# Kernel optimization log

Measured on AMD Instinct MI355X. Metric: run time of the kernel, lower is better.

The kernel has to match this reference:

```python
import jax, jax.numpy as jnp
import numpy as np

D_MODEL = 1024
NUM_HEADS = 16
HEAD_DIM = D_MODEL // NUM_HEADS


def setup_inputs() -> dict:
    key = jax.random.key(0)
    ks = jax.random.split(key, 9)
    B, S, D = 4, 2048, D_MODEL
    scale = 1.0 / np.sqrt(D)
    x = jax.random.normal(ks[0], (B, S, D), dtype=jnp.float32)
    wq = jax.random.normal(ks[1], (D, D), dtype=jnp.float32) * scale
    wk = jax.random.normal(ks[2], (D, D), dtype=jnp.float32) * scale
    wv = jax.random.normal(ks[3], (D, D), dtype=jnp.float32) * scale
    wo = jax.random.normal(ks[4], (D, D), dtype=jnp.float32) * scale
    bq = jax.random.normal(ks[5], (D,), dtype=jnp.float32) * 0.02
    bk = jax.random.normal(ks[6], (D,), dtype=jnp.float32) * 0.02
    bv = jax.random.normal(ks[7], (D,), dtype=jnp.float32) * 0.02
    bo = jax.random.normal(ks[8], (D,), dtype=jnp.float32) * 0.02
    return {"x": x, "wq": wq, "bq": bq, "wk": wk, "bk": bk,
            "wv": wv, "bv": bv, "wo": wo, "bo": bo}


def _split_heads(t):  # [B,S,D] -> [B,H,S,Dh]
    B, S, _ = t.shape
    return t.reshape(B, S, NUM_HEADS, HEAD_DIM).transpose(0, 2, 1, 3)


def reference(x, wq, bq, wk, bk, wv, bv, wo, bo):
    B, S, D = x.shape
    q = _split_heads(x @ wq + bq)  # [B,H,S,Dh]
    k = _split_heads(x @ wk + bk)
    v = _split_heads(x @ wv + bv)
    scores = jnp.einsum("bhqd,bhkd->bhqk", q, k) / jnp.sqrt(
        jnp.asarray(HEAD_DIM, dtype=x.dtype))
    causal = jnp.tril(jnp.ones((S, S), dtype=bool))  # [S,S]
    scores = jnp.where(causal, scores, jnp.finfo(scores.dtype).min)
    attn = jax.nn.softmax(scores, axis=-1)
    ctx = jnp.einsum("bhqk,bhkd->bhqd", attn, v)  # [B,H,S,Dh]
    ctx = ctx.transpose(0, 2, 1, 3).reshape(B, S, D)
    return ctx @ wo + bo
```

## Files before the change

### kernel.cpp

```cpp
#include <hip/hip_runtime.h>
#include <hip/hip_bf16.h>
#include <stdint.h>

#define DMODEL 1024
#define NH 16
#define DH 64
#define BATCH 4
#define SEQ 2048

#if __has_builtin(__builtin_amdgcn_exp2f)
#define EXP2F(x) __builtin_amdgcn_exp2f(x)
#else
#define EXP2F(x) exp2f(x)
#endif

typedef __attribute__((ext_vector_type(8))) short short8;
typedef __attribute__((ext_vector_type(4))) float f32x4;
typedef __attribute__((ext_vector_type(4))) ushort ushort4v;

__device__ __forceinline__ ushort f2bf(float f) {
    union { float f; unsigned u; } v; v.f = f;
    unsigned r = v.u + 0x7fffu + ((v.u >> 16) & 1u);
    return (ushort)(r >> 16);
}

__global__ __launch_bounds__(256) void convert_bf16(const float* __restrict__ src,
                                                    ushort* __restrict__ dst) {
    const size_t i = ((size_t)blockIdx.x * 256 + threadIdx.x) * 8;
    float4 a = *(const float4*)(src + i);
    float4 b = *(const float4*)(src + i + 4);
    short8 r;
    r[0] = (short)f2bf(a.x); r[1] = (short)f2bf(a.y);
    r[2] = (short)f2bf(a.z); r[3] = (short)f2bf(a.w);
    r[4] = (short)f2bf(b.x); r[5] = (short)f2bf(b.y);
    r[6] = (short)f2bf(b.z); r[7] = (short)f2bf(b.w);
    *(short8*)(dst + i) = r;
}

__global__ __launch_bounds__(256) void transpose_cvt_w4(
    const float* __restrict__ s0, const float* __restrict__ s1,
    const float* __restrict__ s2, const float* __restrict__ s3,
    ushort* __restrict__ d0, ushort* __restrict__ d1,
    ushort* __restrict__ d2, ushort* __restrict__ d3) {
    __shared__ ushort tile[64][65];
    const int z = blockIdx.z;
    const float* src = (z == 0) ? s0 : (z == 1) ? s1 : (z == 2) ? s2 : s3;
    ushort* dst = (z == 0) ? d0 : (z == 1) ? d1 : (z == 2) ? d2 : d3;
    const int bx = blockIdx.x * 64;
    const int by = blockIdx.y * 64;
    const int tx = threadIdx.x & 63, ty = threadIdx.x >> 6;
    #pragma unroll
    for (int i = 0; i < 64; i += 4)
        tile[ty + i][tx] = f2bf(src[(size_t)(by + ty + i) * DMODEL + bx + tx]);
    __syncthreads();
    #pragma unroll
    for (int i = 0; i < 64; i += 4)
        dst[(size_t)(bx + ty + i) * DMODEL + by + tx] = tile[tx][ty + i];
}

#define BK 64
#define NT 16

template <int MODE>
__global__ __launch_bounds__(512, 2) void gemm_tile(
    const ushort* __restrict__ A, const ushort* __restrict__ Bt,
    const float* __restrict__ b0, const float* __restrict__ b1,
    const float* __restrict__ b2,
    void* __restrict__ o0v, void* __restrict__ o1v, void* __restrict__ o2v) {
    __shared__ __align__(16) ushort lds[73728];
    const int tid  = threadIdx.x;
    const int lane = tid & 63;
    const int wv   = tid >> 6;

    const int bid = blockIdx.x;
    const int by  = 4 * (bid & 7) + ((bid >> 3) & 3);
    const int bx  = bid >> 5;
    const int mBase = by * 256, nBase = bx * 128;

    const int wm = (wv >> 1) * 64;
    const int wn = (wv & 1) * 64;
    const int frow = lane & 15;
    const int fq   = lane >> 4;
    const int r7   = frow & 7;
    const int sw0  = (fq ^ r7) << 3;
    const int sw1  = ((4 + fq) ^ r7) << 3;

    const int trow = tid >> 3;
    const int tcho = ((tid & 7) ^ (trow & 7)) * 8;
    const ushort* gA = A  + (size_t)(mBase + trow) * DMODEL + tcho;
    const ushort* gB = Bt + (size_t)(nBase + trow) * DMODEL + tcho;
    const int ldsw = wv * 512;

    f32x4 acc[4][4];
    #pragma unroll
    for (int i = 0; i < 4; ++i)
        #pragma unroll
        for (int j = 0; j < 4; ++j) acc[i][j] = (f32x4){0.f, 0.f, 0.f, 0.f};

#define STG(gp, off) __builtin_amdgcn_global_load_lds( \
    (const __attribute__((address_space(1))) void*)(gp), \
    (__attribute__((address_space(3))) void*)&lds[(off) + ldsw], 16, 0, 0)
#define STAGE_A(sb, u, h) STG(gA + (size_t)(h) * 64 * DMODEL + (u) * BK, \
                              (sb) + (h) * 4096)
#define STAGE_B(sb, u, h) STG(gB + (size_t)(h) * 64 * DMODEL + (u) * BK, \
                              (sb) + 16384 + (h) * 4096)

    STAGE_A(0, 0, 0); STAGE_A(0, 0, 1); STAGE_A(0, 0, 2); STAGE_A(0, 0, 3);
    STAGE_B(0, 0, 0); STAGE_B(0, 0, 1);
    STAGE_A(24576, 1, 0); STAGE_A(24576, 1, 1); STAGE_A(24576, 1, 2);
    STAGE_A(24576, 1, 3); STAGE_B(24576, 1, 0); STAGE_B(24576, 1, 1);
    asm volatile("s_waitcnt vmcnt(6)" ::: "memory");
    __builtin_amdgcn_s_barrier();

    int sc = 0;
    #pragma unroll 1
    for (int u = 0; u < NT; ++u) {
        const int scB = sc * 24576;
        const int sp  = (sc == 0) ? 2 : sc - 1;
        const int spB = sp * 24576;
        const ushort* bufA = &lds[scB + wm * 64];
        const ushort* bufB = &lds[scB + 16384 + wn * 64];

        short8 af[4][2], bf[2][2];

        #pragma unroll
        for (int f = 0; f < 4; ++f) {
            const int ro = (f * 16 + frow) * 64;
            af[f][0] = *(const short8*)&bufA[ro + sw0];
            af[f][1] = *(const short8*)&bufA[ro + sw1];
        }
        #pragma unroll
        for (int f2 = 0; f2 < 2; ++f2) {
            const int ro = (f2 * 16 + frow) * 64;
            bf[f2][0] = *(const short8*)&bufB[ro + sw0];
            bf[f2][1] = *(const short8*)&bufB[ro + sw1];
        }
        if (u + 2 < NT) {
            STAGE_A(spB, u + 2, 0); STAGE_A(spB, u + 2, 1); STAGE_A(spB, u + 2, 2);
        }
        __builtin_amdgcn_s_barrier();
        asm volatile("s_waitcnt lgkmcnt(0)" ::: "memory");
        __builtin_amdgcn_s_setprio(1);
        #pragma unroll
        for (int f = 0; f < 4; ++f)
            #pragma unroll
            for (int f2 = 0; f2 < 2; ++f2)
                #pragma unroll
                for (int ks = 0; ks < 2; ++ks)
                    acc[f][f2] = __builtin_amdgcn_mfma_f32_16x16x32_bf16(
                        af[f][ks], bf[f2][ks], acc[f][f2], 0, 0, 0);
        __builtin_amdgcn_s_setprio(0);
        __builtin_amdgcn_s_barrier();

        #pragma unroll
        for (int f2 = 0; f2 < 2; ++f2) {
            const int ro = (32 + f2 * 16 + frow) * 64;
            bf[f2][0] = *(const short8*)&bufB[ro + sw0];
            bf[f2][1] = *(const short8*)&bufB[ro + sw1];
        }
        if (u + 2 < NT) {
            STAGE_A(spB, u + 2, 3); STAGE_B(spB, u + 2, 0); STAGE_B(spB, u + 2, 1);
        }
        __builtin_amdgcn_s_barrier();
        asm volatile("s_waitcnt lgkmcnt(0)" ::: "memory");
        __builtin_amdgcn_s_setprio(1);
        #pragma unroll
        for (int f = 0; f < 4; ++f)
            #pragma unroll
            for (int f2 = 0; f2 < 2; ++f2)
                #pragma unroll
                for (int ks = 0; ks < 2; ++ks)
                    acc[f][2 + f2] = __builtin_amdgcn_mfma_f32_16x16x32_bf16(
                        af[f][ks], bf[f2][ks], acc[f][2 + f2], 0, 0, 0);
        __builtin_amdgcn_s_setprio(0);
        if (u + 2 < NT)       { asm volatile("s_waitcnt vmcnt(6)" ::: "memory"); }
        else if (u + 2 == NT) { asm volatile("s_waitcnt vmcnt(0)" ::: "memory"); }
        __builtin_amdgcn_s_barrier();
        sc = (sc == 2) ? 0 : sc + 1;
    }
#undef STG
#undef STAGE_A
#undef STAGE_B

    const int orow = fq * 4;
    const int ocol = frow;

    if (MODE == 1) {
        #pragma unroll
        for (int i = 0; i < 4; ++i)
            #pragma unroll
            for (int j = 0; j < 4; ++j)
                #pragma unroll
                for (int r = 0; r < 4; ++r) {
                    const int m = mBase + wm + i * 16 + orow + r;
                    const int n = nBase + wn + j * 16 + ocol;
                    ((float*)o0v)[(size_t)m * DMODEL + n] = acc[i][j][r] + b0[n];
                }
        return;
    }

    __syncthreads();
    ushort* o0 = (ushort*)o0v; ushort* o1 = (ushort*)o1v; ushort* o2 = (ushort*)o2v;
    ushort* sw = &lds[wv * 1152];
    const int mat = nBase >> 10;
    const int nb0 = (nBase & 1023) + wn;
    const int hb  = nb0 >> 6;
    const float* bp = (mat == 0) ? b0 : ((mat == 1) ? b1 : b2);
    float bj[4];
    #pragma unroll
    for (int j = 0; j < 4; ++j) bj[j] = bp[nb0 + j * 16 + ocol];
    const int mrow = mBase + wm;
    const int bbq = mrow >> 11;
    const int s0w = mrow & 2047;
    const float qscale = (mat == 0) ? 0.1803368801f : 1.0f;

    if (mat < 2) {
        ushort* obase = ((mat == 0) ? o0 : o1) +
                        ((size_t)(bbq * NH + hb) * SEQ + s0w) * DH;
        const int row = lane >> 2, cc = lane & 3;
        #pragma unroll
        for (int i = 0; i < 4; ++i) {
            #pragma unroll
            for (int j = 0; j < 4; ++j)
                #pragma unroll
                for (int r = 0; r < 4; ++r)
                    sw[(orow + r) * 72 + j * 16 + ocol] =
                        f2bf((acc[i][j][r] + bj[j]) * qscale);
            asm volatile("s_waitcnt lgkmcnt(0)" ::: "memory");
            #pragma unroll
            for (int p = 0; p < 2; ++p) {
                short8 v8 = *(const short8*)&sw[row * 72 + cc * 8 + p * 32];
                *(short8*)&obase[(size_t)(i * 16 + row) * DH + cc * 8 + p * 32] = v8;
            }
            asm volatile("s_waitcnt lgkmcnt(0)" ::: "memory");
        }
    } else {
        const int rowd = lane >> 2, scl = lane & 3;
        #pragma unroll
        for (int j = 0; j < 4; ++j) {
            #pragma unroll
            for (int ii = 0; ii < 4; ++ii)
                #pragma unroll
                for (int r = 0; r < 4; ++r)
                    sw[ocol * 72 + ii * 16 + orow + r] = f2bf(acc[ii][j][r] + bj[j]);
            asm volatile("s_waitcnt lgkmcnt(0)" ::: "memory");
            ushort* vbase = o2 + ((size_t)(bbq * NH + hb) * DH + j * 16 + rowd) * SEQ + s0w;
            #pragma unroll
            for (int p = 0; p < 2; ++p) {
                short8 v8 = *(const short8*)&sw[rowd * 72 + scl * 8 + p * 32];
                *(short8*)&vbase[scl * 8 + p * 32] = v8;
            }
            asm volatile("s_waitcnt lgkmcnt(0)" ::: "memory");
        }
    }
}

#define PSTR 72
__global__ __launch_bounds__(512, 6) void flash_attn(
    const ushort* __restrict__ Q, const ushort* __restrict__ K,
    const ushort* __restrict__ Vt, ushort* __restrict__ ctx) {
    __shared__ __align__(16) ushort Ks[2][4096];
    __shared__ __align__(16) ushort Vs[2][4096];
    __shared__ __align__(16) ushort plds[8][16 * PSTR];
    const int tid  = threadIdx.x;
    const int lane = tid & 63;
    const int wv   = tid >> 6;
    const int bh   = blockIdx.x & 63;
    const int Jp   = blockIdx.x >> 6;
    const int bb = bh >> 4, h = bh & 15;

    const ushort* Qb = Q + (size_t)bh * SEQ * DH;
    const ushort* Kb = K + (size_t)bh * SEQ * DH;
    const ushort* Vb = Vt + (size_t)bh * DH * SEQ;

    const int frow = lane & 15;
    const int fq   = lane >> 4;
    const int trow = tid >> 3;
    const int tcho = ((tid & 7) ^ (trow & 7)) * 8;
    const int ldsw = wv * 512;

    short8 ones;
    #pragma unroll
    for (int i = 0; i < 8; ++i) ones[i] = (short)0x3F80;

#define FA_STG(gp, lp) __builtin_amdgcn_global_load_lds( \
    (const __attribute__((address_space(1))) void*)(gp), \
    (__attribute__((address_space(3))) void*)(lp), 16, 0, 0)

    #pragma unroll 1
    for (int half = 0; half < 2; ++half) {
        const int J = half ? (15 - Jp) : Jp;
        const int ktmax = 2 * J + 1;
        const int q0 = J * 128 + (wv >> 2) * 64 + (wv & 3) * 16;
        const int qmax = q0 + 15;

        short8 qf[2];
        #pragma unroll
        for (int ks = 0; ks < 2; ++ks)
            qf[ks] = *(const short8*)&Qb[(size_t)(q0 + frow) * DH + ks * 32 + fq * 8];

        f32x4 o[4], lacc;
        #pragma unroll
        for (int t = 0; t < 4; ++t) o[t] = (f32x4){0.f, 0.f, 0.f, 0.f};
        lacc = (f32x4){0.f, 0.f, 0.f, 0.f};

        FA_STG(Kb + (size_t)trow * DH + tcho, &Ks[0][ldsw]);
        FA_STG(Vb + (size_t)trow * SEQ + tcho, &Vs[0][ldsw]);
        asm volatile("s_waitcnt vmcnt(0)" ::: "memory");
        __builtin_amdgcn_s_barrier();

        #pragma unroll 1
        for (int kt = 0; kt <= ktmax; ++kt) {
            const int k0 = kt * 64;
            const int cur = kt & 1;
            if (kt < ktmax) {
                const int kn = k0 + 64;
                FA_STG(Kb + (size_t)(kn + trow) * DH + tcho, &Ks[cur ^ 1][ldsw]);
                FA_STG(Vb + (size_t)trow * SEQ + kn + tcho, &Vs[cur ^ 1][ldsw]);
            }
            const ushort* Ksc = Ks[cur];
            const ushort* Vsc = Vs[cur];

            if (k0 <= qmax) {
            if (k0 + 64 <= q0) {
                f32x4 sacc[4];
                #pragma unroll
                for (int nt = 0; nt < 4; ++nt) sacc[nt] = (f32x4){0.f, 0.f, 0.f, 0.f};
                #pragma unroll
                for (int nt = 0; nt < 4; ++nt) {
                    const int row = nt * 16 + frow, r7 = row & 7;
                    #pragma unroll
                    for (int ks = 0; ks < 2; ++ks) {
                        short8 kf = *(const short8*)
                            &Ksc[(row >> 3) * 512 + r7 * 64 + (((ks * 4 + fq) ^ r7) * 8)];
                        sacc[nt] = __builtin_amdgcn_mfma_f32_16x16x32_bf16(kf, qf[ks],
                                                                          sacc[nt], 0, 0, 0);
                    }
                }
                #pragma unroll
                for (int nt = 0; nt < 4; ++nt) {
                    float p0 = EXP2F(sacc[nt][0]);
                    float p1 = EXP2F(sacc[nt][1]);
                    float p2 = EXP2F(sacc[nt][2]);
                    float p3 = EXP2F(sacc[nt][3]);
                    uint2 dw;
                    dw.x = __builtin_amdgcn_perm(__float_as_uint(p1), __float_as_uint(p0),
                                                 0x07060302u);
                    dw.y = __builtin_amdgcn_perm(__float_as_uint(p3), __float_as_uint(p2),
                                                 0x07060302u);
                    *(uint2*)&plds[wv][frow * PSTR + nt * 16 + fq * 4] = dw;
                }
                asm volatile("s_waitcnt lgkmcnt(0)" ::: "memory");
                #pragma unroll
                for (int kc = 0; kc < 2; ++kc) {
                    short8 pf = *(const short8*)&plds[wv][frow * PSTR + kc * 32 + fq * 8];
                    lacc = __builtin_amdgcn_mfma_f32_16x16x32_bf16(ones, pf, lacc, 0, 0, 0);
                    __builtin_amdgcn_s_setprio(1);
                    #pragma unroll
                    for (int t = 0; t < 4; ++t) {
                        const int row = t * 16 + frow, r7 = row & 7;
                        short8 vf = *(const short8*)
                            &Vsc[(row >> 3) * 512 + r7 * 64 + (((kc * 4 + fq) ^ r7) * 8)];
                        o[t] = __builtin_amdgcn_mfma_f32_16x16x32_bf16(vf, pf, o[t], 0, 0, 0);
                    }
                    __builtin_amdgcn_s_setprio(0);
                }
            } else {
                const int qrow = q0 + frow;
                f32x4 sacc[4];
                #pragma unroll
                for (int nt = 0; nt < 4; ++nt) sacc[nt] = (f32x4){0.f, 0.f, 0.f, 0.f};
                #pragma unroll
                for (int nt = 0; nt < 4; ++nt)
                    if (k0 + nt * 16 <= qmax) {
                        const int row = nt * 16 + frow, r7 = row & 7;
                        #pragma unroll
                        for (int ks = 0; ks < 2; ++ks) {
                            short8 kf = *(const short8*)
                                &Ksc[(row >> 3) * 512 + r7 * 64 + (((ks * 4 + fq) ^ r7) * 8)];
                            sacc[nt] = __builtin_amdgcn_mfma_f32_16x16x32_bf16(kf, qf[ks],
                                                                              sacc[nt], 0, 0, 0);
                        }
                    }
                #pragma unroll
                for (int nt = 0; nt < 4; ++nt) {
                    uint2 dw; dw.x = 0u; dw.y = 0u;
                    if (k0 + nt * 16 <= qmax) {
                        float pp[4];
                        #pragma unroll
                        for (int r = 0; r < 4; ++r) {
                            const float e = EXP2F(sacc[nt][r]);
                            pp[r] = (k0 + nt * 16 + fq * 4 + r <= qrow) ? e : 0.f;
                        }
                        dw.x = __builtin_amdgcn_perm(__float_as_uint(pp[1]),
                                                     __float_as_uint(pp[0]), 0x07060302u);
                        dw.y = __builtin_amdgcn_perm(__float_as_uint(pp[3]),
                                                     __float_as_uint(pp[2]), 0x07060302u);
                    }
                    *(uint2*)&plds[wv][frow * PSTR + nt * 16 + fq * 4] = dw;
                }
                asm volatile("s_waitcnt lgkmcnt(0)" ::: "memory");
                #pragma unroll
                for (int kc = 0; kc < 2; ++kc) {
                    if (k0 + kc * 32 <= qmax) {
                        short8 pf = *(const short8*)&plds[wv][frow * PSTR + kc * 32 + fq * 8];
                        lacc = __builtin_amdgcn_mfma_f32_16x16x32_bf16(ones, pf, lacc, 0, 0, 0);
                        #pragma unroll
                        for (int t = 0; t < 4; ++t) {
                            const int row = t * 16 + frow, r7 = row & 7;
                            short8 vf = *(const short8*)
                                &Vsc[(row >> 3) * 512 + r7 * 64 + (((kc * 4 + fq) ^ r7) * 8)];
                            o[t] = __builtin_amdgcn_mfma_f32_16x16x32_bf16(vf, pf, o[t], 0, 0, 0);
                        }
                    }
                }
            }
            }

            asm volatile("s_waitcnt lgkmcnt(0) vmcnt(0)" ::: "memory");
            __builtin_amdgcn_s_barrier();
        }

        const float inv = 1.0f / lacc[0];
        const int qrow = q0 + frow;
        ushort* cp = ctx + (size_t)(bb * SEQ + qrow) * DMODEL + h * DH;
        #pragma unroll
        for (int t = 0; t < 4; ++t) {
            ushort4v ov;
            #pragma unroll
            for (int r = 0; r < 4; ++r) ov[r] = f2bf(o[t][r] * inv);
            *(ushort4v*)&cp[t * 16 + fq * 4] = ov;
        }
    }
#undef FA_STG
}

extern "C" void kernel_launch(void* const* d_in, const int* in_sizes, int n_in,
                              void* d_out, int out_size, void* d_ws, size_t ws_size,
                              hipStream_t stream) {
    const float* x  = (const float*)d_in[0];
    const float* wq = (const float*)d_in[1];
    const float* bq = (const float*)d_in[2];
    const float* wk = (const float*)d_in[3];
    const float* bk = (const float*)d_in[4];
    const float* wvp = (const float*)d_in[5];
    const float* bv = (const float*)d_in[6];
    const float* wo = (const float*)d_in[7];
    const float* bo = (const float*)d_in[8];
    float* out = (float*)d_out;
    ushort* ws = (ushort*)d_ws;

    const size_t QSZ = (size_t)BATCH * NH * SEQ * DH;
    ushort* xbf   = ws;
    ushort* qws   = ws + QSZ;
    ushort* kws   = ws + 2 * QSZ;
    ushort* vtws  = ws + 3 * QSZ;
    ushort* ctxws = ws + 4 * QSZ;
    ushort* wtqkv = ws + 5 * QSZ;
    ushort* wto   = wtqkv + 3 * (size_t)DMODEL * DMODEL;

    dim3 tb(256);
    convert_bf16<<<dim3(4096), tb, 0, stream>>>(x, xbf);
    transpose_cvt_w4<<<dim3(16, 16, 4), tb, 0, stream>>>(
        wq, wk, wvp, wo,
        wtqkv, wtqkv + (size_t)DMODEL * DMODEL, wtqkv + 2 * (size_t)DMODEL * DMODEL, wto);

    gemm_tile<0><<<dim3(768), dim3(512), 0, stream>>>(xbf, wtqkv, bq, bk, bv,
                                                      qws, kws, vtws);
    flash_attn<<<dim3(512), dim3(512), 0, stream>>>(qws, kws, vtws, ctxws);
    gemm_tile<1><<<dim3(256), dim3(512), 0, stream>>>(ctxws, wto, bo, nullptr, nullptr,
                                                      out, nullptr, nullptr);
}
```

Baseline: 232.9 us.

## Collapse two-phase GEMM main loop into a single-phase schedule

Replaces the two half-iterations of the triple-buffered GEMM loop (each loading half the B fragments, issuing half the global stages, and fencing with barriers and lgkmcnt waits) with one phase. All six global-to-LDS stages are issued up front, all four B fragments are loaded, and 32 MFMAs run back to back. This removes two barriers and explicit LDS waits per iteration, meant to cut synchronization stalls. In exchange it holds more fragment registers and drops the interleaving of memory issue with compute.

```diff
diff --git a/kernel.cpp b/kernel.cpp
--- a/kernel.cpp
+++ b/kernel.cpp
@@ -121,8 +121,13 @@
         const ushort* bufA = &lds[scB + wm * 64];
         const ushort* bufB = &lds[scB + 16384 + wn * 64];
 
-        short8 af[4][2], bf[2][2];
-
+        if (u + 2 < NT) {
+            STAGE_A(spB, u + 2, 0); STAGE_A(spB, u + 2, 1);
+            STAGE_A(spB, u + 2, 2); STAGE_A(spB, u + 2, 3);
+            STAGE_B(spB, u + 2, 0); STAGE_B(spB, u + 2, 1);
+        }
+
+        short8 af[4][2], bf[4][2];
         #pragma unroll
         for (int f = 0; f < 4; ++f) {
             const int ro = (f * 16 + frow) * 64;
@@ -130,49 +135,22 @@
             af[f][1] = *(const short8*)&bufA[ro + sw1];
         }
         #pragma unroll
-        for (int f2 = 0; f2 < 2; ++f2) {
-            const int ro = (f2 * 16 + frow) * 64;
-            bf[f2][0] = *(const short8*)&bufB[ro + sw0];
-            bf[f2][1] = *(const short8*)&bufB[ro + sw1];
-        }
-        if (u + 2 < NT) {
-            STAGE_A(spB, u + 2, 0); STAGE_A(spB, u + 2, 1); STAGE_A(spB, u + 2, 2);
-        }
-        __builtin_amdgcn_s_barrier();
-        asm volatile("s_waitcnt lgkmcnt(0)" ::: "memory");
+        for (int j = 0; j < 4; ++j) {
+            const int ro = (j * 16 + frow) * 64;
+            bf[j][0] = *(const short8*)&bufB[ro + sw0];
+            bf[j][1] = *(const short8*)&bufB[ro + sw1];
+        }
         __builtin_amdgcn_s_setprio(1);
         #pragma unroll
         for (int f = 0; f < 4; ++f)
             #pragma unroll
-            for (int f2 = 0; f2 < 2; ++f2)
+            for (int j = 0; j < 4; ++j)
                 #pragma unroll
                 for (int ks = 0; ks < 2; ++ks)
-                    acc[f][f2] = __builtin_amdgcn_mfma_f32_16x16x32_bf16(
-                        af[f][ks], bf[f2][ks], acc[f][f2], 0, 0, 0);
+                    acc[f][j] = __builtin_amdgcn_mfma_f32_16x16x32_bf16(
+                        af[f][ks], bf[j][ks], acc[f][j], 0, 0, 0);
         __builtin_amdgcn_s_setprio(0);
-        __builtin_amdgcn_s_barrier();
-
-        #pragma unroll
-        for (int f2 = 0; f2 < 2; ++f2) {
-            const int ro = (32 + f2 * 16 + frow) * 64;
-            bf[f2][0] = *(const short8*)&bufB[ro + sw0];
-            bf[f2][1] = *(const short8*)&bufB[ro + sw1];
-        }
-        if (u + 2 < NT) {
-            STAGE_A(spB, u + 2, 3); STAGE_B(spB, u + 2, 0); STAGE_B(spB, u + 2, 1);
-        }
-        __builtin_amdgcn_s_barrier();
-        asm volatile("s_waitcnt lgkmcnt(0)" ::: "memory");
-        __builtin_amdgcn_s_setprio(1);
-        #pragma unroll
-        for (int f = 0; f < 4; ++f)
-            #pragma unroll
-            for (int f2 = 0; f2 < 2; ++f2)
-                #pragma unroll
-                for (int ks = 0; ks < 2; ++ks)
-                    acc[f][2 + f2] = __builtin_amdgcn_mfma_f32_16x16x32_bf16(
-                        af[f][ks], bf[f2][ks], acc[f][2 + f2], 0, 0, 0);
-        __builtin_amdgcn_s_setprio(0);
+
         if (u + 2 < NT)       { asm volatile("s_waitcnt vmcnt(6)" ::: "memory"); }
         else if (u + 2 == NT) { asm volatile("s_waitcnt vmcnt(0)" ::: "memory"); }
         __builtin_amdgcn_s_barrier();
```

Measured after the change: 242.5 us. 4.1% more time.
